# Kernel tuning notes

Measured on AMD Instinct MI355X. Metric: run time of the kernel, lower is better.

The kernel has to match this reference:

```python
import jax, jax.numpy as jnp
import numpy as np

N, E, D, H = 50000, 800000, 128, 4
EPS = 1e-5


def setup_inputs() -> dict:
    key = jax.random.key(0)
    ks = jax.random.split(key, 12)
    s_in = 1.0 / np.sqrt(D)
    s_att = 1.0 / np.sqrt(D)
    inp = {
        "x": jax.random.normal(ks[0], (N, D), dtype=jnp.float32),
        "edge_index": jax.random.randint(ks[1], (2, E), 0, N, dtype=jnp.int32),
        # conv1 params: W [D, H*D], att_src/att_dst [H, D], bias [D]
        "W1": jax.random.normal(ks[2], (D, H * D), dtype=jnp.float32) * s_in,
        "as1": jax.random.normal(ks[3], (H, D), dtype=jnp.float32) * s_att,
        "ad1": jax.random.normal(ks[4], (H, D), dtype=jnp.float32) * s_att,
        "b1": jnp.zeros((D,), dtype=jnp.float32),
        "g1": jnp.ones((D,), dtype=jnp.float32),
        "be1": jnp.zeros((D,), dtype=jnp.float32),
        # conv2 params
        "W2": jax.random.normal(ks[5], (D, H * D), dtype=jnp.float32) * s_in,
        "as2": jax.random.normal(ks[6], (H, D), dtype=jnp.float32) * s_att,
        "ad2": jax.random.normal(ks[7], (H, D), dtype=jnp.float32) * s_att,
        "b2": jnp.zeros((D,), dtype=jnp.float32),
        "g2": jnp.ones((D,), dtype=jnp.float32),
        "be2": jnp.zeros((D,), dtype=jnp.float32),
    }
    return inp


def _gat_conv(x, src, dst, W, att_src, att_dst, bias):
    # project: [N, H, C]
    h = (x @ W).reshape(N, H, D)
    a_src = jnp.einsum("nhc,hc->nh", h, att_src)  # [N, H]
    a_dst = jnp.einsum("nhc,hc->nh", h, att_dst)  # [N, H]
    # attention logits per edge, softmax over incoming edges of each dst
    logits = jax.nn.leaky_relu(a_src[src] + a_dst[dst], negative_slope=0.2)  # [Etot, H]
    lmax = jax.ops.segment_max(logits, dst, num_segments=N)  # [N, H]
    p = jnp.exp(logits - lmax[dst])
    denom = jax.ops.segment_sum(p, dst, num_segments=N)  # [N, H]
    alpha = p / denom[dst]  # self-loops guarantee denom > 0
    # weighted scatter-add aggregation
    msg = h[src] * alpha[:, :, None]  # [Etot, H, C]
    out = jax.ops.segment_sum(msg, dst, num_segments=N)  # [N, H, C]
    return out.mean(axis=1) + bias  # concat=False: mean over heads


def _batchnorm_relu(x, gamma, beta):
    mu = x.mean(axis=0)
    var = x.var(axis=0)  # biased, as torch uses for normalization
    xn = (x - mu) * jax.lax.rsqrt(var + EPS)
    return jax.nn.relu(xn * gamma + beta)


def reference(x, edge_index, W1, as1, ad1, b1, g1, be1, W2, as2, ad2, b2, g2, be2):
    # add self loops (GATConv default add_self_loops=True)
    loop = jnp.arange(N, dtype=edge_index.dtype)
    src = jnp.concatenate([edge_index[0], loop])
    dst = jnp.concatenate([edge_index[1], loop])
    x = _batchnorm_relu(_gat_conv(x, src, dst, W1, as1, ad1, b1), g1, be1)
    x = _batchnorm_relu(_gat_conv(x, src, dst, W2, as2, ad2, b2), g2, be2)
    return x
```

## Files before the change

kernel.cpp:

```cpp
#include <hip/hip_runtime.h>
#include <hip/hip_bf16.h>
#include <hip/hip_fp16.h>
#include <math.h>

#define NN 50000
#define NP 50048
#define NE 800000
#define ET (NE + NN)
#define DF 128
#define NH 4
#define HD 512
#define BN_EPS 1e-5f

typedef __hip_bfloat16 bf16;
typedef __attribute__((ext_vector_type(8))) short bf16x8;
typedef __attribute__((ext_vector_type(4))) float f32x4;

struct alignas(8) h2x2 { __half2 a, b; };

__global__ __launch_bounds__(256) void cvt_x_bf16(const float* __restrict__ in, bf16* __restrict__ out) {
    int i = blockIdx.x * 256 + threadIdx.x;
    if (i >= NN * DF / 4) return;
    float4 v = reinterpret_cast<const float4*>(in)[i];
    union { bf16 b[4]; short4 s; } u;
    u.b[0] = __float2bfloat16(v.x); u.b[1] = __float2bfloat16(v.y);
    u.b[2] = __float2bfloat16(v.z); u.b[3] = __float2bfloat16(v.w);
    reinterpret_cast<short4*>(out)[i] = u.s;
}

__global__ __launch_bounds__(256) void make_wsd(const float* __restrict__ W1, const float* __restrict__ as1,
                                                const float* __restrict__ ad1,
                                                const float* __restrict__ W2, const float* __restrict__ as2,
                                                const float* __restrict__ ad2,
                                                float* __restrict__ wsd) {
    int t = blockIdx.x * 256 + threadIdx.x;
    if (t >= 2048) return;
    int layer = t >> 10;
    int o = (t >> 7) & 7;
    int d = t & 127;
    int h = o & 3;
    const float* W  = layer ? W2 : W1;
    const float* av = layer ? (o < 4 ? as2 : ad2) : (o < 4 ? as1 : ad1);
    const float* wrow = W + d * HD + h * DF;
    const float* arow = av + h * DF;
    float sum = 0.f;
    for (int c = 0; c < DF; ++c) sum += wrow[c] * arow[c];
    wsd[layer * 1024 + o * DF + d] = sum;
}

__global__ __launch_bounds__(256) void cvt_bt2(const float* __restrict__ W1, const float* __restrict__ W2,
                                               bf16* __restrict__ B1, bf16* __restrict__ B2) {
    int i = blockIdx.x * 256 + threadIdx.x;
    if (i >= 2 * DF * HD) return;
    int layer = i >> 16;
    int ii = i & 65535;
    int c = ii >> 9, k = ii & 511;
    int h = k >> 7, d = k & 127;
    const float* W = layer ? W2 : W1;
    bf16* B = layer ? B2 : B1;
    B[ii] = __float2bfloat16(0.25f * W[d * HD + h * DF + c]);
}

__global__ __launch_bounds__(256) void xscore(const bf16* __restrict__ X,
                                              const float* __restrict__ wsd,
                                              float* __restrict__ a_src,
                                              float* __restrict__ a_dst) {
    __shared__ float w[8][DF];
    reinterpret_cast<float4*>(&w[0][0])[threadIdx.x] = reinterpret_cast<const float4*>(wsd)[threadIdx.x];
    __syncthreads();
    const int n = blockIdx.x * 4 + (threadIdx.x >> 6);
    const int l = threadIdx.x & 63;
    unsigned xv = reinterpret_cast<const unsigned*>(X)[n * 64 + l];
    float x0 = __uint_as_float(xv << 16);
    float x1 = __uint_as_float(xv & 0xffff0000u);
    float v[8];
    #pragma unroll
    for (int o = 0; o < 8; ++o)
        v[o] = x0 * w[o][2 * l] + x1 * w[o][2 * l + 1];
    #pragma unroll
    for (int off = 1; off < 64; off <<= 1) {
        #pragma unroll
        for (int o = 0; o < 8; ++o) v[o] += __shfl_xor(v[o], off);
    }
    if (l == 0) {
        reinterpret_cast<float4*>(a_src)[n] = make_float4(v[0], v[1], v[2], v[3]);
        reinterpret_cast<float4*>(a_dst)[n] = make_float4(v[4], v[5], v[6], v[7]);
    }
}

__global__ __launch_bounds__(256) void count_rank(const int* __restrict__ ei, int* __restrict__ counts,
                                                  int* __restrict__ rank) {
    int e = (blockIdx.x * 256 + threadIdx.x) * 2;
    if (e >= ET) return;
    int d0, d1;
    if (e + 1 < NE) {
        int2 dd = *reinterpret_cast<const int2*>(ei + NE + e);
        d0 = dd.x; d1 = dd.y;
    } else {
        d0 = (e < NE) ? ei[NE + e] : (e - NE);
        d1 = (e + 1 < NE) ? ei[NE + e + 1] : (e + 1 - NE);
    }
    rank[e]     = atomicAdd(&counts[d0 << 4], 1);
    rank[e + 1] = atomicAdd(&counts[d1 << 4], 1);
}

__global__ __launch_bounds__(256) void scan1(const int* __restrict__ counts, int* __restrict__ bsum) {
    __shared__ int sd[256];
    int i = blockIdx.x * 256 + threadIdx.x;
    sd[threadIdx.x] = (i < NN) ? counts[i << 4] : 0;
    __syncthreads();
    for (int s = 128; s > 0; s >>= 1) {
        if (threadIdx.x < s) sd[threadIdx.x] += sd[threadIdx.x + s];
        __syncthreads();
    }
    if (threadIdx.x == 0) bsum[blockIdx.x] = sd[0];
}

__global__ __launch_bounds__(256) void scan2(int* __restrict__ bsum, int nb) {
    __shared__ int sd[256];
    int i = threadIdx.x;
    int v = (i < nb) ? bsum[i] : 0;
    sd[i] = v;
    __syncthreads();
    for (int s = 1; s < 256; s <<= 1) {
        int t = sd[i];
        int u = (i >= s) ? sd[i - s] : 0;
        __syncthreads();
        sd[i] = t + u;
        __syncthreads();
    }
    if (i < nb) bsum[i] = sd[i] - v;
}

__global__ __launch_bounds__(256) void scan3(const int* __restrict__ counts, const int* __restrict__ bsum,
                                             int* __restrict__ row_ptr) {
    __shared__ int sd[256];
    int i = blockIdx.x * 256 + threadIdx.x;
    int v = (i < NN) ? counts[i << 4] : 0;
    sd[threadIdx.x] = v;
    __syncthreads();
    for (int s = 1; s < 256; s <<= 1) {
        int t = sd[threadIdx.x];
        int u = (threadIdx.x >= s) ? sd[threadIdx.x - s] : 0;
        __syncthreads();
        sd[threadIdx.x] = t + u;
        __syncthreads();
    }
    int excl = sd[threadIdx.x] - v + bsum[blockIdx.x];
    if (i < NN) row_ptr[i] = excl;
    if (i == 0) row_ptr[NN] = ET;
}

__global__ __launch_bounds__(256) void fill_scatter(const int* __restrict__ ei, const int* __restrict__ rank,
                                                    const int* __restrict__ row_ptr, int* __restrict__ col) {
    int e = (blockIdx.x * 256 + threadIdx.x) * 2;
    if (e >= ET) return;
    int s0, d0, s1, d1;
    if (e + 1 < NE) {
        int2 ss = *reinterpret_cast<const int2*>(ei + e);
        int2 dd = *reinterpret_cast<const int2*>(ei + NE + e);
        s0 = ss.x; s1 = ss.y; d0 = dd.x; d1 = dd.y;
    } else {
        if (e < NE) { s0 = ei[e]; d0 = ei[NE + e]; } else { s0 = d0 = e - NE; }
        if (e + 1 < NE) { s1 = ei[e + 1]; d1 = ei[NE + e + 1]; } else { s1 = d1 = e + 1 - NE; }
    }
    int2 rk = *reinterpret_cast<const int2*>(rank + e);
    col[row_ptr[d0] + rk.x] = s0;
    col[row_ptr[d1] + rk.y] = s1;
}

__global__ __launch_bounds__(256) void edge_alpha(const float* __restrict__ a_src,
                                                  const float* __restrict__ a_dst,
                                                  const int* __restrict__ row_ptr,
                                                  const int* __restrict__ col,
                                                  __half* __restrict__ alpha) {
    const int n = blockIdx.x * 4 + (threadIdx.x >> 6);
    const int l = threadIdx.x & 63;
    const int start = row_ptr[n], end = row_ptr[n + 1];
    const float4 ad4 = reinterpret_cast<const float4*>(a_dst)[n];
    const float4* __restrict__ as4 = reinterpret_cast<const float4*>(a_src);
    if (end - start <= 64) {
        const int j = start + l;
        float lv[4] = {-1e30f, -1e30f, -1e30f, -1e30f};
        if (j < end) {
            float4 a = as4[col[j]];
            lv[0] = a.x + ad4.x; lv[1] = a.y + ad4.y; lv[2] = a.z + ad4.z; lv[3] = a.w + ad4.w;
            #pragma unroll
            for (int h = 0; h < 4; ++h) lv[h] = lv[h] > 0.f ? lv[h] : 0.2f * lv[h];
        }
        float m[4], p[4], s[4];
        #pragma unroll
        for (int h = 0; h < 4; ++h) m[h] = lv[h];
        #pragma unroll
        for (int off = 1; off < 64; off <<= 1) {
            #pragma unroll
            for (int h = 0; h < 4; ++h) m[h] = fmaxf(m[h], __shfl_xor(m[h], off));
        }
        #pragma unroll
        for (int h = 0; h < 4; ++h) { p[h] = (j < end) ? __expf(lv[h] - m[h]) : 0.f; s[h] = p[h]; }
        #pragma unroll
        for (int off = 1; off < 64; off <<= 1) {
            #pragma unroll
            for (int h = 0; h < 4; ++h) s[h] += __shfl_xor(s[h], off);
        }
        if (j < end) {
            h2x2 o;
            o.a = __floats2half2_rn(p[0] / s[0], p[1] / s[1]);
            o.b = __floats2half2_rn(p[2] / s[2], p[3] / s[3]);
            reinterpret_cast<h2x2*>(alpha)[j] = o;
        }
    } else {
        float m[4] = {-1e30f, -1e30f, -1e30f, -1e30f}, s[4] = {0.f, 0.f, 0.f, 0.f};
        for (int base = start; base < end; base += 64) {
            const int j = base + l;
            float lv[4] = {-1e30f, -1e30f, -1e30f, -1e30f};
            if (j < end) {
                float4 a = as4[col[j]];
                lv[0] = a.x + ad4.x; lv[1] = a.y + ad4.y; lv[2] = a.z + ad4.z; lv[3] = a.w + ad4.w;
                #pragma unroll
                for (int h = 0; h < 4; ++h) lv[h] = lv[h] > 0.f ? lv[h] : 0.2f * lv[h];
            }
            float cm[4], cp[4];
            #pragma unroll
            for (int h = 0; h < 4; ++h) cm[h] = lv[h];
            #pragma unroll
            for (int off = 1; off < 64; off <<= 1) {
                #pragma unroll
                for (int h = 0; h < 4; ++h) cm[h] = fmaxf(cm[h], __shfl_xor(cm[h], off));
            }
            #pragma unroll
            for (int h = 0; h < 4; ++h) {
                float nm = fmaxf(m[h], cm[h]);
                cp[h] = (j < end) ? __expf(lv[h] - nm) : 0.f;
                s[h] *= __expf(m[h] - nm);
                m[h] = nm;
            }
            #pragma unroll
            for (int off = 1; off < 64; off <<= 1) {
                #pragma unroll
                for (int h = 0; h < 4; ++h) cp[h] += __shfl_xor(cp[h], off);
            }
            #pragma unroll
            for (int h = 0; h < 4; ++h) s[h] += cp[h];
        }
        for (int base = start; base < end; base += 64) {
            const int j = base + l;
            if (j < end) {
                float4 a = as4[col[j]];
                float v0 = a.x + ad4.x, v1 = a.y + ad4.y, v2 = a.z + ad4.z, v3 = a.w + ad4.w;
                v0 = v0 > 0.f ? v0 : 0.2f * v0; v1 = v1 > 0.f ? v1 : 0.2f * v1;
                v2 = v2 > 0.f ? v2 : 0.2f * v2; v3 = v3 > 0.f ? v3 : 0.2f * v3;
                h2x2 o;
                o.a = __floats2half2_rn(__expf(v0 - m[0]) / s[0], __expf(v1 - m[1]) / s[1]);
                o.b = __floats2half2_rn(__expf(v2 - m[2]) / s[2], __expf(v3 - m[3]) / s[3]);
                reinterpret_cast<h2x2*>(alpha)[j] = o;
            }
        }
    }
}

#define EDGE(xu, pu) {                                                               \
    float lo = __uint_as_float((xu) << 16);                                          \
    float hi = __uint_as_float((xu) & 0xffff0000u);                                  \
    float2 f01 = __half22float2(*reinterpret_cast<const __half2*>(&(pu).x));         \
    float2 f23 = __half22float2(*reinterpret_cast<const __half2*>(&(pu).y));         \
    acc[0][0] += f01.x * lo; acc[0][1] += f01.x * hi;                                \
    acc[1][0] += f01.y * lo; acc[1][1] += f01.y * hi;                                \
    acc[2][0] += f23.x * lo; acc[2][1] += f23.x * hi;                                \
    acc[3][0] += f23.y * lo; acc[3][1] += f23.y * hi; }

__global__ __launch_bounds__(256) void aggregate_x(const bf16* __restrict__ X,
                                                   const __half* __restrict__ alpha,
                                                   const int* __restrict__ row_ptr,
                                                   const int* __restrict__ col,
                                                   bf16* __restrict__ aggX) {
    const int n = blockIdx.x * 4 + (threadIdx.x >> 6);
    const int l = threadIdx.x & 63;
    const int start = row_ptr[n], end = row_ptr[n + 1];
    const unsigned* __restrict__ X4 = reinterpret_cast<const unsigned*>(X);
    float acc[4][2] = {};
    int j = start;
    for (; j + 4 <= end; j += 4) {
        int c0 = col[j], c1 = col[j + 1], c2 = col[j + 2], c3 = col[j + 3];
        unsigned x0 = X4[c0 * 64 + l];
        unsigned x1 = X4[c1 * 64 + l];
        unsigned x2 = X4[c2 * 64 + l];
        unsigned x3 = X4[c3 * 64 + l];
        uint2 p0 = *reinterpret_cast<const uint2*>(alpha + 4 * j);
        uint2 p1 = *reinterpret_cast<const uint2*>(alpha + 4 * (j + 1));
        uint2 p2 = *reinterpret_cast<const uint2*>(alpha + 4 * (j + 2));
        uint2 p3 = *reinterpret_cast<const uint2*>(alpha + 4 * (j + 3));
        EDGE(x0, p0) EDGE(x1, p1) EDGE(x2, p2) EDGE(x3, p3)
    }
    for (; j < end; ++j) {
        unsigned x0 = X4[col[j] * 64 + l];
        uint2 p0 = *reinterpret_cast<const uint2*>(alpha + 4 * j);
        EDGE(x0, p0)
    }
    unsigned* outp = reinterpret_cast<unsigned*>(aggX) + (size_t)n * 256;
    #pragma unroll
    for (int h = 0; h < 4; ++h) {
        union { bf16 b; unsigned short u; } plo, phi;
        plo.b = __float2bfloat16(acc[h][0]);
        phi.b = __float2bfloat16(acc[h][1]);
        outp[h * 64 + l] = (unsigned)plo.u | ((unsigned)phi.u << 16);
    }
}

__global__ __launch_bounds__(256) void gemm_out(const bf16* __restrict__ A,
                                                const bf16* __restrict__ Bt,
                                                const float* __restrict__ bias,
                                                bf16* __restrict__ outb,
                                                float* __restrict__ stats, int M) {
    __shared__ __align__(16) char Bs[65536];
    __shared__ float ssum[128], ssq[128];
    const int tid = threadIdx.x;
    if (tid < 128) { ssum[tid] = 0.f; ssq[tid] = 0.f; }
    const int m0 = blockIdx.x * 64;
    const char* Ab = (const char*)A + (size_t)m0 * 1024;
    const char* Bb = (const char*)Bt;
    auto stageB = [&](int ph) {
        #pragma unroll
        for (int i = 0; i < 16; ++i) {
            int d = (tid + i * 256) * 16;
            int c = d >> 9;
            int kb = d & 511;
            int src = c * 1024 + ph * 512 + (kb ^ ((c & 7) << 4));
            __builtin_amdgcn_global_load_lds(
                (const __attribute__((address_space(1))) void*)(Bb + src),
                (__attribute__((address_space(3))) void*)(Bs + d), 16, 0, 0);
        }
    };
    const int lane = tid & 63;
    const int wave = tid >> 6;
    const int wm = (wave & 1) * 32;
    const int wnb = (wave >> 1) * 64;
    const int lr = lane & 15;
    const int lkb = (lane >> 4) * 16;
    f32x4 acc[2][4] = {};
    const char* arow0 = Ab + (size_t)(wm + lr) * 1024 + lkb;
    const char* arow1 = Ab + (size_t)(wm + 16 + lr) * 1024 + lkb;
    stageB(0);
    #pragma unroll
    for (int ph = 0; ph < 2; ++ph) {
        __syncthreads();
        #pragma unroll 4
        for (int kk = 0; kk < 8; ++kk) {
            int kg = ph * 512 + kk * 64;
            bf16x8 a0 = *(const bf16x8*)(arow0 + kg);
            bf16x8 a1 = *(const bf16x8*)(arow1 + kg);
            int kb = kk * 64 + lkb;
            #pragma unroll
            for (int nf = 0; nf < 4; ++nf) {
                int c = wnb + nf * 16 + lr;
                bf16x8 b = *(const bf16x8*)(Bs + c * 512 + (kb ^ ((c & 7) << 4)));
                acc[0][nf] = __builtin_amdgcn_mfma_f32_16x16x32_bf16(a0, b, acc[0][nf], 0, 0, 0);
                acc[1][nf] = __builtin_amdgcn_mfma_f32_16x16x32_bf16(a1, b, acc[1][nf], 0, 0, 0);
            }
        }
        if (ph == 0) {
            __syncthreads();
            stageB(1);
        }
    }
    const int orow = (lane >> 4) * 4;
    float bcol[4];
    #pragma unroll
    for (int nf = 0; nf < 4; ++nf) bcol[nf] = bias[wnb + nf * 16 + lr];
    #pragma unroll
    for (int nf = 0; nf < 4; ++nf) {
        float cs = 0.f, cq = 0.f;
        int c = wnb + nf * 16 + lr;
        #pragma unroll
        for (int mi = 0; mi < 2; ++mi) {
            #pragma unroll
            for (int r = 0; r < 4; ++r) {
                int gr = m0 + wm + mi * 16 + orow + r;
                if (gr < M) {
                    float v = acc[mi][nf][r] + bcol[nf];
                    outb[(size_t)gr * DF + c] = __float2bfloat16(v);
                    cs += v; cq += v * v;
                }
            }
        }
        atomicAdd(&ssum[c], cs);
        atomicAdd(&ssq[c], cq);
    }
    __syncthreads();
    if (tid < 128) {
        atomicAdd(&stats[tid], ssum[tid]);
        atomicAdd(&stats[128 + tid], ssq[tid]);
    }
}

__device__ __forceinline__ void bn_core(const uint4 v, int c0, const float* stats,
                                        const float* gamma, const float* beta, float* o) {
    float xv[8];
    xv[0] = __uint_as_float(v.x << 16); xv[1] = __uint_as_float(v.x & 0xffff0000u);
    xv[2] = __uint_as_float(v.y << 16); xv[3] = __uint_as_float(v.y & 0xffff0000u);
    xv[4] = __uint_as_float(v.z << 16); xv[5] = __uint_as_float(v.z & 0xffff0000u);
    xv[6] = __uint_as_float(v.w << 16); xv[7] = __uint_as_float(v.w & 0xffff0000u);
    #pragma unroll
    for (int k = 0; k < 8; ++k) {
        int c = c0 + k;
        float mu = stats[c] * (1.f / NN);
        float var = stats[128 + c] * (1.f / NN) - mu * mu;
        o[k] = fmaxf((xv[k] - mu) * rsqrtf(var + BN_EPS) * gamma[c] + beta[c], 0.f);
    }
}

__global__ __launch_bounds__(256) void bn_apply_bf16(const bf16* __restrict__ x, const float* __restrict__ stats,
                                                     const float* __restrict__ gamma, const float* __restrict__ beta,
                                                     bf16* __restrict__ out) {
    int i = blockIdx.x * 256 + threadIdx.x;
    if (i >= NN * DF / 8) return;
    uint4 v = reinterpret_cast<const uint4*>(x)[i];
    float o[8];
    bn_core(v, (i * 8) & 127, stats, gamma, beta, o);
    uint4 w;
    unsigned short* wb = reinterpret_cast<unsigned short*>(&w);
    #pragma unroll
    for (int k = 0; k < 8; ++k) {
        union { bf16 b; unsigned short u; } t;
        t.b = __float2bfloat16(o[k]);
        wb[k] = t.u;
    }
    reinterpret_cast<uint4*>(out)[i] = w;
}

__global__ __launch_bounds__(256) void bn_apply_f32(const bf16* __restrict__ x, const float* __restrict__ stats,
                                                    const float* __restrict__ gamma, const float* __restrict__ beta,
                                                    float* __restrict__ out) {
    int i = blockIdx.x * 256 + threadIdx.x;
    if (i >= NN * DF / 8) return;
    uint4 v = reinterpret_cast<const uint4*>(x)[i];
    float o[8];
    bn_core(v, (i * 8) & 127, stats, gamma, beta, o);
    float4* op = reinterpret_cast<float4*>(out) + (size_t)i * 2;
    op[0] = make_float4(o[0], o[1], o[2], o[3]);
    op[1] = make_float4(o[4], o[5], o[6], o[7]);
}

extern "C" void kernel_launch(void* const* d_in, const int* in_sizes, int n_in,
                              void* d_out, int out_size, void* d_ws, size_t ws_size,
                              hipStream_t stream) {
    (void)in_sizes; (void)n_in; (void)out_size; (void)ws_size;
    const float* x   = (const float*)d_in[0];
    const int*   ei  = (const int*)d_in[1];
    const float* W1  = (const float*)d_in[2];
    const float* as1 = (const float*)d_in[3];
    const float* ad1 = (const float*)d_in[4];
    const float* b1  = (const float*)d_in[5];
    const float* g1  = (const float*)d_in[6];
    const float* be1 = (const float*)d_in[7];
    const float* W2  = (const float*)d_in[8];
    const float* as2 = (const float*)d_in[9];
    const float* ad2 = (const float*)d_in[10];
    const float* b2  = (const float*)d_in[11];
    const float* g2  = (const float*)d_in[12];
    const float* be2 = (const float*)d_in[13];
    float* out = (float*)d_out;

    char* ws = (char*)d_ws;
    size_t off = 0;
    auto alloc = [&](size_t bytes) -> void* {
        void* p = ws + off;
        off += (bytes + 255) & ~(size_t)255;
        return p;
    };
    bf16*   aggX    = (bf16*)alloc((size_t)NP * HD * 2);
    bf16*   xb      = (bf16*)alloc((size_t)NP * DF * 2);
    bf16*   Bt2a    = (bf16*)alloc((size_t)DF * HD * 2);
    bf16*   Bt2b    = (bf16*)alloc((size_t)DF * HD * 2);
    float*  wsd     = (float*)alloc(2 * 1024 * 4);
    float*  a_src   = (float*)alloc((size_t)NN * NH * 4);
    float*  a_dst   = (float*)alloc((size_t)NN * NH * 4);
    int*    row_ptr = (int*)alloc((size_t)(NN + 1) * 4);
    int*    bsum    = (int*)alloc(256 * 4);
    int*    colidx  = (int*)alloc((size_t)ET * 4);
    __half* alpha   = (__half*)alloc((size_t)ET * 8);
    bf16*   agg     = (bf16*)alloc((size_t)NN * DF * 2);
    float*  stats   = (float*)alloc(256 * 4);
    int*    counts  = (int*)agg;
    int*    rank    = (int*)((char*)agg + ((size_t)NP << 6));

    const int NB = (NN + 255) / 256;
    const int EB2 = (ET / 2 + 255) / 256;
    const int BNB = (NN * DF / 8 + 255) / 256;

    cvt_x_bf16<<<(NN * DF / 4 + 255) / 256, 256, 0, stream>>>(x, xb);
    make_wsd<<<8, 256, 0, stream>>>(W1, as1, ad1, W2, as2, ad2, wsd);
    cvt_bt2<<<(2 * DF * HD + 255) / 256, 256, 0, stream>>>(W1, W2, Bt2a, Bt2b);
    hipMemsetAsync(counts, 0, (size_t)NP << 6, stream);
    count_rank<<<EB2, 256, 0, stream>>>(ei, counts, rank);
    scan1<<<NB, 256, 0, stream>>>(counts, bsum);
    scan2<<<1, 256, 0, stream>>>(bsum, NB);
    scan3<<<NB, 256, 0, stream>>>(counts, bsum, row_ptr);
    fill_scatter<<<EB2, 256, 0, stream>>>(ei, rank, row_ptr, colidx);

    xscore<<<NN / 4, 256, 0, stream>>>(xb, wsd, a_src, a_dst);
    edge_alpha<<<NN / 4, 256, 0, stream>>>(a_src, a_dst, row_ptr, colidx, alpha);
    aggregate_x<<<NN / 4, 256, 0, stream>>>(xb, alpha, row_ptr, colidx, aggX);
    hipMemsetAsync(stats, 0, 256 * 4, stream);
    gemm_out<<<NP / 64, 256, 0, stream>>>(aggX, Bt2a, b1, agg, stats, NN);
    bn_apply_bf16<<<BNB, 256, 0, stream>>>(agg, stats, g1, be1, xb);

    xscore<<<NN / 4, 256, 0, stream>>>(xb, wsd + 1024, a_src, a_dst);
    edge_alpha<<<NN / 4, 256, 0, stream>>>(a_src, a_dst, row_ptr, colidx, alpha);
    aggregate_x<<<NN / 4, 256, 0, stream>>>(xb, alpha, row_ptr, colidx, aggX);
    hipMemsetAsync(stats, 0, 256 * 4, stream);
    gemm_out<<<NP / 64, 256, 0, stream>>>(aggX, Bt2b, b2, agg, stats, NN);
    bn_apply_f32<<<BNB, 256, 0, stream>>>(agg, stats, g2, be2, out);
}
```

Measured before the change: 390.4 us.

## Fuse edge softmax into aggregation with online softmax, drop alpha buffer

Merges the edge_alpha and aggregate_x kernels into one kernel. It computes attention logits per 64-edge chunk, keeps an online softmax with running max and sum, and accumulates weighted neighbor features in registers. Normalization happens once at the end. The lane layout changes to four edge groups of 16 lanes, each loading 16-byte feature vectors, which adds a cross-group shuffle reduction. It also folds the stats memset into xscore. The fused kernel removes the fp16 alpha round-trip and a kernel launch, at the cost of more registers (32 accumulators) and serialized per-edge inner loops that may reduce memory-level parallelism.

```diff
diff --git a/kernel.cpp b/kernel.cpp
--- a/kernel.cpp
+++ b/kernel.cpp
@@ -1,6 +1,5 @@
 #include <hip/hip_runtime.h>
 #include <hip/hip_bf16.h>
-#include <hip/hip_fp16.h>
 #include <math.h>
 
 #define NN 50000
@@ -15,8 +14,6 @@
 typedef __hip_bfloat16 bf16;
 typedef __attribute__((ext_vector_type(8))) short bf16x8;
 typedef __attribute__((ext_vector_type(4))) float f32x4;
-
-struct alignas(8) h2x2 { __half2 a, b; };
 
 __global__ __launch_bounds__(256) void cvt_x_bf16(const float* __restrict__ in, bf16* __restrict__ out) {
     int i = blockIdx.x * 256 + threadIdx.x;
@@ -64,7 +61,10 @@
 __global__ __launch_bounds__(256) void xscore(const bf16* __restrict__ X,
                                               const float* __restrict__ wsd,
                                               float* __restrict__ a_src,
-                                              float* __restrict__ a_dst) {
+                                              float* __restrict__ a_dst,
+                                              float* __restrict__ stats) {
+    if (blockIdx.x == 0 && threadIdx.x < 64)
+        reinterpret_cast<float4*>(stats)[threadIdx.x] = make_float4(0.f, 0.f, 0.f, 0.f);
     __shared__ float w[8][DF];
     reinterpret_cast<float4*>(&w[0][0])[threadIdx.x] = reinterpret_cast<const float4*>(wsd)[threadIdx.x];
     __syncthreads();
@@ -169,141 +169,109 @@
     col[row_ptr[d1] + rk.y] = s1;
 }
 
-__global__ __launch_bounds__(256) void edge_alpha(const float* __restrict__ a_src,
-                                                  const float* __restrict__ a_dst,
-                                                  const int* __restrict__ row_ptr,
-                                                  const int* __restrict__ col,
-                                                  __half* __restrict__ alpha) {
-    const int n = blockIdx.x * 4 + (threadIdx.x >> 6);
+__global__ __launch_bounds__(256) void agg_fused(const bf16* __restrict__ X,
+                                                 const float* __restrict__ a_src,
+                                                 const float* __restrict__ a_dst,
+                                                 const int* __restrict__ row_ptr,
+                                                 const int* __restrict__ col,
+                                                 bf16* __restrict__ aggX) {
+    __shared__ __align__(16) float4 pal[4][64];
+    __shared__ int pcol[4][64];
+    const int w = threadIdx.x >> 6;
+    const int n = blockIdx.x * 4 + w;
     const int l = threadIdx.x & 63;
+    const int g = l >> 4;
+    const int q = l & 15;
     const int start = row_ptr[n], end = row_ptr[n + 1];
     const float4 ad4 = reinterpret_cast<const float4*>(a_dst)[n];
     const float4* __restrict__ as4 = reinterpret_cast<const float4*>(a_src);
-    if (end - start <= 64) {
-        const int j = start + l;
+    const uint4* __restrict__ X16 = reinterpret_cast<const uint4*>(X);
+    float m[4] = {-1e30f, -1e30f, -1e30f, -1e30f};
+    float s[4] = {0.f, 0.f, 0.f, 0.f};
+    float acc[4][8] = {};
+    for (int base = start; base < end; base += 64) {
+        const int j = base + l;
+        const bool valid = j < end;
+        const int cj = valid ? col[j] : 0;
         float lv[4] = {-1e30f, -1e30f, -1e30f, -1e30f};
-        if (j < end) {
-            float4 a = as4[col[j]];
+        if (valid) {
+            float4 a = as4[cj];
             lv[0] = a.x + ad4.x; lv[1] = a.y + ad4.y; lv[2] = a.z + ad4.z; lv[3] = a.w + ad4.w;
             #pragma unroll
             for (int h = 0; h < 4; ++h) lv[h] = lv[h] > 0.f ? lv[h] : 0.2f * lv[h];
         }
-        float m[4], p[4], s[4];
-        #pragma unroll
-        for (int h = 0; h < 4; ++h) m[h] = lv[h];
+        float cm[4];
+        #pragma unroll
+        for (int h = 0; h < 4; ++h) cm[h] = lv[h];
         #pragma unroll
         for (int off = 1; off < 64; off <<= 1) {
             #pragma unroll
-            for (int h = 0; h < 4; ++h) m[h] = fmaxf(m[h], __shfl_xor(m[h], off));
-        }
-        #pragma unroll
-        for (int h = 0; h < 4; ++h) { p[h] = (j < end) ? __expf(lv[h] - m[h]) : 0.f; s[h] = p[h]; }
+            for (int h = 0; h < 4; ++h) cm[h] = fmaxf(cm[h], __shfl_xor(cm[h], off));
+        }
+        float p[4], ps[4];
+        #pragma unroll
+        for (int h = 0; h < 4; ++h) {
+            float nm = fmaxf(m[h], cm[h]);
+            float sc = __expf(m[h] - nm);
+            p[h] = valid ? __expf(lv[h] - nm) : 0.f;
+            s[h] *= sc;
+            #pragma unroll
+            for (int f = 0; f < 8; ++f) acc[h][f] *= sc;
+            m[h] = nm;
+            ps[h] = p[h];
+        }
         #pragma unroll
         for (int off = 1; off < 64; off <<= 1) {
             #pragma unroll
-            for (int h = 0; h < 4; ++h) s[h] += __shfl_xor(s[h], off);
-        }
-        if (j < end) {
-            h2x2 o;
-            o.a = __floats2half2_rn(p[0] / s[0], p[1] / s[1]);
-            o.b = __floats2half2_rn(p[2] / s[2], p[3] / s[3]);
-            reinterpret_cast<h2x2*>(alpha)[j] = o;
-        }
-    } else {
-        float m[4] = {-1e30f, -1e30f, -1e30f, -1e30f}, s[4] = {0.f, 0.f, 0.f, 0.f};
-        for (int base = start; base < end; base += 64) {
-            const int j = base + l;
-            float lv[4] = {-1e30f, -1e30f, -1e30f, -1e30f};
-            if (j < end) {
-                float4 a = as4[col[j]];
-                lv[0] = a.x + ad4.x; lv[1] = a.y + ad4.y; lv[2] = a.z + ad4.z; lv[3] = a.w + ad4.w;
-                #pragma unroll
-                for (int h = 0; h < 4; ++h) lv[h] = lv[h] > 0.f ? lv[h] : 0.2f * lv[h];
+            for (int h = 0; h < 4; ++h) ps[h] += __shfl_xor(ps[h], off);
+        }
+        #pragma unroll
+        for (int h = 0; h < 4; ++h) s[h] += ps[h];
+        pal[w][l] = make_float4(p[0], p[1], p[2], p[3]);
+        pcol[w][l] = cj;
+        __builtin_amdgcn_wave_barrier();
+        const int cnt = min(64, end - base);
+        for (int ee = 0; ee < cnt; ee += 4) {
+            int cc = pcol[w][ee + g];
+            float4 pa = pal[w][ee + g];
+            uint4 xv = X16[(size_t)cc * 16 + q];
+            float xf[8];
+            xf[0] = __uint_as_float(xv.x << 16); xf[1] = __uint_as_float(xv.x & 0xffff0000u);
+            xf[2] = __uint_as_float(xv.y << 16); xf[3] = __uint_as_float(xv.y & 0xffff0000u);
+            xf[4] = __uint_as_float(xv.z << 16); xf[5] = __uint_as_float(xv.z & 0xffff0000u);
+            xf[6] = __uint_as_float(xv.w << 16); xf[7] = __uint_as_float(xv.w & 0xffff0000u);
+            #pragma unroll
+            for (int f = 0; f < 8; ++f) {
+                acc[0][f] += pa.x * xf[f];
+                acc[1][f] += pa.y * xf[f];
+                acc[2][f] += pa.z * xf[f];
+                acc[3][f] += pa.w * xf[f];
             }
-            float cm[4], cp[4];
-            #pragma unroll
-            for (int h = 0; h < 4; ++h) cm[h] = lv[h];
-            #pragma unroll
-            for (int off = 1; off < 64; off <<= 1) {
-                #pragma unroll
-                for (int h = 0; h < 4; ++h) cm[h] = fmaxf(cm[h], __shfl_xor(cm[h], off));
+        }
+        __builtin_amdgcn_wave_barrier();
+    }
+    #pragma unroll
+    for (int h = 0; h < 4; ++h)
+        #pragma unroll
+        for (int f = 0; f < 8; ++f) {
+            acc[h][f] += __shfl_xor(acc[h][f], 16);
+            acc[h][f] += __shfl_xor(acc[h][f], 32);
+        }
+    if (l < 16) {
+        uint4* outp = reinterpret_cast<uint4*>(aggX) + (size_t)n * 64;
+        #pragma unroll
+        for (int h = 0; h < 4; ++h) {
+            float inv = 1.f / s[h];
+            uint4 wv;
+            unsigned short* wb = reinterpret_cast<unsigned short*>(&wv);
+            #pragma unroll
+            for (int f = 0; f < 8; ++f) {
+                union { bf16 b; unsigned short u; } t;
+                t.b = __float2bfloat16(acc[h][f] * inv);
+                wb[f] = t.u;
             }
-            #pragma unroll
-            for (int h = 0; h < 4; ++h) {
-                float nm = fmaxf(m[h], cm[h]);
-                cp[h] = (j < end) ? __expf(lv[h] - nm) : 0.f;
-                s[h] *= __expf(m[h] - nm);
-                m[h] = nm;
-            }
-            #pragma unroll
-            for (int off = 1; off < 64; off <<= 1) {
-                #pragma unroll
-                for (int h = 0; h < 4; ++h) cp[h] += __shfl_xor(cp[h], off);
-            }
-            #pragma unroll
-            for (int h = 0; h < 4; ++h) s[h] += cp[h];
-        }
-        for (int base = start; base < end; base += 64) {
-            const int j = base + l;
-            if (j < end) {
-                float4 a = as4[col[j]];
-                float v0 = a.x + ad4.x, v1 = a.y + ad4.y, v2 = a.z + ad4.z, v3 = a.w + ad4.w;
-                v0 = v0 > 0.f ? v0 : 0.2f * v0; v1 = v1 > 0.f ? v1 : 0.2f * v1;
-                v2 = v2 > 0.f ? v2 : 0.2f * v2; v3 = v3 > 0.f ? v3 : 0.2f * v3;
-                h2x2 o;
-                o.a = __floats2half2_rn(__expf(v0 - m[0]) / s[0], __expf(v1 - m[1]) / s[1]);
-                o.b = __floats2half2_rn(__expf(v2 - m[2]) / s[2], __expf(v3 - m[3]) / s[3]);
-                reinterpret_cast<h2x2*>(alpha)[j] = o;
-            }
-        }
-    }
-}
-
-#define EDGE(xu, pu) {                                                               \
-    float lo = __uint_as_float((xu) << 16);                                          \
-    float hi = __uint_as_float((xu) & 0xffff0000u);                                  \
-    float2 f01 = __half22float2(*reinterpret_cast<const __half2*>(&(pu).x));         \
-    float2 f23 = __half22float2(*reinterpret_cast<const __half2*>(&(pu).y));         \
-    acc[0][0] += f01.x * lo; acc[0][1] += f01.x * hi;                                \
-    acc[1][0] += f01.y * lo; acc[1][1] += f01.y * hi;                                \
-    acc[2][0] += f23.x * lo; acc[2][1] += f23.x * hi;                                \
-    acc[3][0] += f23.y * lo; acc[3][1] += f23.y * hi; }
-
-__global__ __launch_bounds__(256) void aggregate_x(const bf16* __restrict__ X,
-                                                   const __half* __restrict__ alpha,
-                                                   const int* __restrict__ row_ptr,
-                                                   const int* __restrict__ col,
-                                                   bf16* __restrict__ aggX) {
-    const int n = blockIdx.x * 4 + (threadIdx.x >> 6);
-    const int l = threadIdx.x & 63;
-    const int start = row_ptr[n], end = row_ptr[n + 1];
-    const unsigned* __restrict__ X4 = reinterpret_cast<const unsigned*>(X);
-    float acc[4][2] = {};
-    int j = start;
-    for (; j + 4 <= end; j += 4) {
-        int c0 = col[j], c1 = col[j + 1], c2 = col[j + 2], c3 = col[j + 3];
-        unsigned x0 = X4[c0 * 64 + l];
-        unsigned x1 = X4[c1 * 64 + l];
-        unsigned x2 = X4[c2 * 64 + l];
-        unsigned x3 = X4[c3 * 64 + l];
-        uint2 p0 = *reinterpret_cast<const uint2*>(alpha + 4 * j);
-        uint2 p1 = *reinterpret_cast<const uint2*>(alpha + 4 * (j + 1));
-        uint2 p2 = *reinterpret_cast<const uint2*>(alpha + 4 * (j + 2));
-        uint2 p3 = *reinterpret_cast<const uint2*>(alpha + 4 * (j + 3));
-        EDGE(x0, p0) EDGE(x1, p1) EDGE(x2, p2) EDGE(x3, p3)
-    }
-    for (; j < end; ++j) {
-        unsigned x0 = X4[col[j] * 64 + l];
-        uint2 p0 = *reinterpret_cast<const uint2*>(alpha + 4 * j);
-        EDGE(x0, p0)
-    }
-    unsigned* outp = reinterpret_cast<unsigned*>(aggX) + (size_t)n * 256;
-    #pragma unroll
-    for (int h = 0; h < 4; ++h) {
-        union { bf16 b; unsigned short u; } plo, phi;
-        plo.b = __float2bfloat16(acc[h][0]);
-        phi.b = __float2bfloat16(acc[h][1]);
-        outp[h * 64 + l] = (unsigned)plo.u | ((unsigned)phi.u << 16);
+            outp[h * 16 + q] = wv;
+        }
     }
 }
 
@@ -478,7 +446,6 @@
     int*    row_ptr = (int*)alloc((size_t)(NN + 1) * 4);
     int*    bsum    = (int*)alloc(256 * 4);
     int*    colidx  = (int*)alloc((size_t)ET * 4);
-    __half* alpha   = (__half*)alloc((size_t)ET * 8);
     bf16*   agg     = (bf16*)alloc((size_t)NN * DF * 2);
     float*  stats   = (float*)alloc(256 * 4);
     int*    counts  = (int*)agg;
@@ -498,17 +465,13 @@
     scan3<<<NB, 256, 0, stream>>>(counts, bsum, row_ptr);
     fill_scatter<<<EB2, 256, 0, stream>>>(ei, rank, row_ptr, colidx);
 
-    xscore<<<NN / 4, 256, 0, stream>>>(xb, wsd, a_src, a_dst);
-    edge_alpha<<<NN / 4, 256, 0, stream>>>(a_src, a_dst, row_ptr, colidx, alpha);
-    aggregate_x<<<NN / 4, 256, 0, stream>>>(xb, alpha, row_ptr, colidx, aggX);
-    hipMemsetAsync(stats, 0, 256 * 4, stream);
+    xscore<<<NN / 4, 256, 0, stream>>>(xb, wsd, a_src, a_dst, stats);
+    agg_fused<<<NN / 4, 256, 0, stream>>>(xb, a_src, a_dst, row_ptr, colidx, aggX);
     gemm_out<<<NP / 64, 256, 0, stream>>>(aggX, Bt2a, b1, agg, stats, NN);
     bn_apply_bf16<<<BNB, 256, 0, stream>>>(agg, stats, g1, be1, xb);
 
-    xscore<<<NN / 4, 256, 0, stream>>>(xb, wsd + 1024, a_src, a_dst);
-    edge_alpha<<<NN / 4, 256, 0, stream>>>(a_src, a_dst, row_ptr, colidx, alpha);
-    aggregate_x<<<NN / 4, 256, 0, stream>>>(xb, alpha, row_ptr, colidx, aggX);
-    hipMemsetAsync(stats, 0, 256 * 4, stream);
+    xscore<<<NN / 4, 256, 0, stream>>>(xb, wsd + 1024, a_src, a_dst, stats);
+    agg_fused<<<NN / 4, 256, 0, stream>>>(xb, a_src, a_dst, row_ptr, colidx, aggX);
     gemm_out<<<NP / 64, 256, 0, stream>>>(aggX, Bt2b, b2, agg, stats, NN);
     bn_apply_f32<<<BNB, 256, 0, stream>>>(agg, stats, g2, be2, out);
 }
```

Measured after the change: 400.5 us. 1.03x slower.

## Fuse conversion/BN into xscore, split GEMM columns, deterministic stats reduction

Applied to the files above, without the earlier changes.

Fuses the fp32-to-bf16 conversion of x into the first score kernel, and fuses layer-1 batchnorm+ReLU into the layer-2 score kernel, removing two elementwise passes over node features. The output GEMM is split across 4 column groups of 32 with a 32 KB B tile per block, which cuts LDS per block and the staging phases and raises the block count. Global stats atomics are replaced by per-block partials in scratch plus a single-block reduction kernel. The single-block reduce adds a serial step of about 800 iterations per thread, and the A tile is now re-read from global once per column group.

```diff
diff --git a/kernel.cpp b/kernel.cpp
--- a/kernel.cpp
+++ b/kernel.cpp
@@ -11,6 +11,7 @@
 #define NH 4
 #define HD 512
 #define BN_EPS 1e-5f
+#define MB 782
 
 typedef __hip_bfloat16 bf16;
 typedef __attribute__((ext_vector_type(8))) short bf16x8;
@@ -18,14 +19,11 @@
 
 struct alignas(8) h2x2 { __half2 a, b; };
 
-__global__ __launch_bounds__(256) void cvt_x_bf16(const float* __restrict__ in, bf16* __restrict__ out) {
-    int i = blockIdx.x * 256 + threadIdx.x;
-    if (i >= NN * DF / 4) return;
-    float4 v = reinterpret_cast<const float4*>(in)[i];
-    union { bf16 b[4]; short4 s; } u;
-    u.b[0] = __float2bfloat16(v.x); u.b[1] = __float2bfloat16(v.y);
-    u.b[2] = __float2bfloat16(v.z); u.b[3] = __float2bfloat16(v.w);
-    reinterpret_cast<short4*>(out)[i] = u.s;
+__device__ __forceinline__ float rbf(float x, unsigned short* bits) {
+    union { bf16 b; unsigned short u; } t;
+    t.b = __float2bfloat16(x);
+    *bits = t.u;
+    return __uint_as_float(((unsigned)t.u) << 16);
 }
 
 __global__ __launch_bounds__(256) void make_wsd(const float* __restrict__ W1, const float* __restrict__ as1,
@@ -61,18 +59,65 @@
     B[ii] = __float2bfloat16(0.25f * W[d * HD + h * DF + c]);
 }
 
-__global__ __launch_bounds__(256) void xscore(const bf16* __restrict__ X,
-                                              const float* __restrict__ wsd,
-                                              float* __restrict__ a_src,
-                                              float* __restrict__ a_dst) {
+__global__ __launch_bounds__(256) void cvt_xscore(const float* __restrict__ X,
+                                                  const float* __restrict__ wsd,
+                                                  bf16* __restrict__ xb,
+                                                  float* __restrict__ a_src,
+                                                  float* __restrict__ a_dst) {
     __shared__ float w[8][DF];
     reinterpret_cast<float4*>(&w[0][0])[threadIdx.x] = reinterpret_cast<const float4*>(wsd)[threadIdx.x];
     __syncthreads();
     const int n = blockIdx.x * 4 + (threadIdx.x >> 6);
     const int l = threadIdx.x & 63;
-    unsigned xv = reinterpret_cast<const unsigned*>(X)[n * 64 + l];
-    float x0 = __uint_as_float(xv << 16);
-    float x1 = __uint_as_float(xv & 0xffff0000u);
+    float2 xv = reinterpret_cast<const float2*>(X)[n * 64 + l];
+    unsigned short u0, u1;
+    float x0 = rbf(xv.x, &u0);
+    float x1 = rbf(xv.y, &u1);
+    reinterpret_cast<unsigned*>(xb)[n * 64 + l] = (unsigned)u0 | ((unsigned)u1 << 16);
+    float v[8];
+    #pragma unroll
+    for (int o = 0; o < 8; ++o)
+        v[o] = x0 * w[o][2 * l] + x1 * w[o][2 * l + 1];
+    #pragma unroll
+    for (int off = 1; off < 64; off <<= 1) {
+        #pragma unroll
+        for (int o = 0; o < 8; ++o) v[o] += __shfl_xor(v[o], off);
+    }
+    if (l == 0) {
+        reinterpret_cast<float4*>(a_src)[n] = make_float4(v[0], v[1], v[2], v[3]);
+        reinterpret_cast<float4*>(a_dst)[n] = make_float4(v[4], v[5], v[6], v[7]);
+    }
+}
+
+__global__ __launch_bounds__(256) void bn_xscore(const bf16* __restrict__ agg,
+                                                 const float* __restrict__ stats,
+                                                 const float* __restrict__ gamma,
+                                                 const float* __restrict__ beta,
+                                                 const float* __restrict__ wsd,
+                                                 bf16* __restrict__ xb,
+                                                 float* __restrict__ a_src,
+                                                 float* __restrict__ a_dst) {
+    __shared__ float w[8][DF];
+    __shared__ float sc[DF], sh[DF];
+    reinterpret_cast<float4*>(&w[0][0])[threadIdx.x] = reinterpret_cast<const float4*>(wsd)[threadIdx.x];
+    if (threadIdx.x < DF) {
+        int c = threadIdx.x;
+        float mu = stats[c] * (1.f / NN);
+        float var = stats[128 + c] * (1.f / NN) - mu * mu;
+        float scale = gamma[c] * rsqrtf(var + BN_EPS);
+        sc[c] = scale;
+        sh[c] = beta[c] - mu * scale;
+    }
+    __syncthreads();
+    const int n = blockIdx.x * 4 + (threadIdx.x >> 6);
+    const int l = threadIdx.x & 63;
+    unsigned u = reinterpret_cast<const unsigned*>(agg)[n * 64 + l];
+    float x0 = fmaxf(__uint_as_float(u << 16) * sc[2 * l] + sh[2 * l], 0.f);
+    float x1 = fmaxf(__uint_as_float(u & 0xffff0000u) * sc[2 * l + 1] + sh[2 * l + 1], 0.f);
+    unsigned short u0, u1;
+    x0 = rbf(x0, &u0);
+    x1 = rbf(x1, &u1);
+    reinterpret_cast<unsigned*>(xb)[n * 64 + l] = (unsigned)u0 | ((unsigned)u1 << 16);
     float v[8];
     #pragma unroll
     for (int o = 0; o < 8; ++o)
@@ -311,121 +356,78 @@
                                                 const bf16* __restrict__ Bt,
                                                 const float* __restrict__ bias,
                                                 bf16* __restrict__ outb,
-                                                float* __restrict__ stats, int M) {
-    __shared__ __align__(16) char Bs[65536];
-    __shared__ float ssum[128], ssq[128];
+                                                float* __restrict__ scratch, int M) {
+    __shared__ __align__(16) char Bs[32768];
+    __shared__ float ssum[32], ssq[32];
     const int tid = threadIdx.x;
-    if (tid < 128) { ssum[tid] = 0.f; ssq[tid] = 0.f; }
+    if (tid < 32) { ssum[tid] = 0.f; ssq[tid] = 0.f; }
     const int m0 = blockIdx.x * 64;
+    const int by = blockIdx.y;
     const char* Ab = (const char*)A + (size_t)m0 * 1024;
-    const char* Bb = (const char*)Bt;
-    auto stageB = [&](int ph) {
-        #pragma unroll
-        for (int i = 0; i < 16; ++i) {
-            int d = (tid + i * 256) * 16;
-            int c = d >> 9;
-            int kb = d & 511;
-            int src = c * 1024 + ph * 512 + (kb ^ ((c & 7) << 4));
-            __builtin_amdgcn_global_load_lds(
-                (const __attribute__((address_space(1))) void*)(Bb + src),
-                (__attribute__((address_space(3))) void*)(Bs + d), 16, 0, 0);
-        }
-    };
+    const char* Bb = (const char*)Bt + (size_t)by * 32768;
+    #pragma unroll
+    for (int i = 0; i < 8; ++i) {
+        int d = (tid + i * 256) * 16;
+        int c = d >> 10;
+        int kb = d & 1023;
+        __builtin_amdgcn_global_load_lds(
+            (const __attribute__((address_space(1))) void*)(Bb + c * 1024 + (kb ^ ((c & 7) << 4))),
+            (__attribute__((address_space(3))) void*)(Bs + d), 16, 0, 0);
+    }
     const int lane = tid & 63;
     const int wave = tid >> 6;
     const int wm = (wave & 1) * 32;
-    const int wnb = (wave >> 1) * 64;
+    const int wn = (wave >> 1) * 16;
     const int lr = lane & 15;
     const int lkb = (lane >> 4) * 16;
-    f32x4 acc[2][4] = {};
+    const int cl = wn + lr;
+    f32x4 acc[2] = {};
     const char* arow0 = Ab + (size_t)(wm + lr) * 1024 + lkb;
     const char* arow1 = Ab + (size_t)(wm + 16 + lr) * 1024 + lkb;
-    stageB(0);
-    #pragma unroll
-    for (int ph = 0; ph < 2; ++ph) {
-        __syncthreads();
-        #pragma unroll 4
-        for (int kk = 0; kk < 8; ++kk) {
-            int kg = ph * 512 + kk * 64;
-            bf16x8 a0 = *(const bf16x8*)(arow0 + kg);
-            bf16x8 a1 = *(const bf16x8*)(arow1 + kg);
-            int kb = kk * 64 + lkb;
-            #pragma unroll
-            for (int nf = 0; nf < 4; ++nf) {
-                int c = wnb + nf * 16 + lr;
-                bf16x8 b = *(const bf16x8*)(Bs + c * 512 + (kb ^ ((c & 7) << 4)));
-                acc[0][nf] = __builtin_amdgcn_mfma_f32_16x16x32_bf16(a0, b, acc[0][nf], 0, 0, 0);
-                acc[1][nf] = __builtin_amdgcn_mfma_f32_16x16x32_bf16(a1, b, acc[1][nf], 0, 0, 0);
+    __syncthreads();
+    #pragma unroll 4
+    for (int kk = 0; kk < 16; ++kk) {
+        int kg = kk * 64;
+        bf16x8 a0 = *(const bf16x8*)(arow0 + kg);
+        bf16x8 a1 = *(const bf16x8*)(arow1 + kg);
+        int kb = kg + lkb;
+        bf16x8 b = *(const bf16x8*)(Bs + cl * 1024 + (kb ^ ((cl & 7) << 4)));
+        acc[0] = __builtin_amdgcn_mfma_f32_16x16x32_bf16(a0, b, acc[0], 0, 0, 0);
+        acc[1] = __builtin_amdgcn_mfma_f32_16x16x32_bf16(a1, b, acc[1], 0, 0, 0);
+    }
+    const int orow = (lane >> 4) * 4;
+    const int gc = by * 32 + cl;
+    const float bc = bias[gc];
+    float cs = 0.f, cq = 0.f;
+    #pragma unroll
+    for (int mi = 0; mi < 2; ++mi) {
+        #pragma unroll
+        for (int r = 0; r < 4; ++r) {
+            int gr = m0 + wm + mi * 16 + orow + r;
+            if (gr < M) {
+                float v = acc[mi][r] + bc;
+                outb[(size_t)gr * DF + gc] = __float2bfloat16(v);
+                cs += v; cq += v * v;
             }
         }
-        if (ph == 0) {
-            __syncthreads();
-            stageB(1);
-        }
-    }
-    const int orow = (lane >> 4) * 4;
-    float bcol[4];
-    #pragma unroll
-    for (int nf = 0; nf < 4; ++nf) bcol[nf] = bias[wnb + nf * 16 + lr];
-    #pragma unroll
-    for (int nf = 0; nf < 4; ++nf) {
-        float cs = 0.f, cq = 0.f;
-        int c = wnb + nf * 16 + lr;
-        #pragma unroll
-        for (int mi = 0; mi < 2; ++mi) {
-            #pragma unroll
-            for (int r = 0; r < 4; ++r) {
-                int gr = m0 + wm + mi * 16 + orow + r;
-                if (gr < M) {
-                    float v = acc[mi][nf][r] + bcol[nf];
-                    outb[(size_t)gr * DF + c] = __float2bfloat16(v);
-                    cs += v; cq += v * v;
-                }
-            }
-        }
-        atomicAdd(&ssum[c], cs);
-        atomicAdd(&ssq[c], cq);
-    }
-    __syncthreads();
-    if (tid < 128) {
-        atomicAdd(&stats[tid], ssum[tid]);
-        atomicAdd(&stats[128 + tid], ssq[tid]);
-    }
-}
-
-__device__ __forceinline__ void bn_core(const uint4 v, int c0, const float* stats,
-                                        const float* gamma, const float* beta, float* o) {
-    float xv[8];
-    xv[0] = __uint_as_float(v.x << 16); xv[1] = __uint_as_float(v.x & 0xffff0000u);
-    xv[2] = __uint_as_float(v.y << 16); xv[3] = __uint_as_float(v.y & 0xffff0000u);
-    xv[4] = __uint_as_float(v.z << 16); xv[5] = __uint_as_float(v.z & 0xffff0000u);
-    xv[6] = __uint_as_float(v.w << 16); xv[7] = __uint_as_float(v.w & 0xffff0000u);
-    #pragma unroll
-    for (int k = 0; k < 8; ++k) {
-        int c = c0 + k;
-        float mu = stats[c] * (1.f / NN);
-        float var = stats[128 + c] * (1.f / NN) - mu * mu;
-        o[k] = fmaxf((xv[k] - mu) * rsqrtf(var + BN_EPS) * gamma[c] + beta[c], 0.f);
-    }
-}
-
-__global__ __launch_bounds__(256) void bn_apply_bf16(const bf16* __restrict__ x, const float* __restrict__ stats,
-                                                     const float* __restrict__ gamma, const float* __restrict__ beta,
-                                                     bf16* __restrict__ out) {
-    int i = blockIdx.x * 256 + threadIdx.x;
-    if (i >= NN * DF / 8) return;
-    uint4 v = reinterpret_cast<const uint4*>(x)[i];
-    float o[8];
-    bn_core(v, (i * 8) & 127, stats, gamma, beta, o);
-    uint4 w;
-    unsigned short* wb = reinterpret_cast<unsigned short*>(&w);
-    #pragma unroll
-    for (int k = 0; k < 8; ++k) {
-        union { bf16 b; unsigned short u; } t;
-        t.b = __float2bfloat16(o[k]);
-        wb[k] = t.u;
-    }
-    reinterpret_cast<uint4*>(out)[i] = w;
+    }
+    atomicAdd(&ssum[cl], cs);
+    atomicAdd(&ssq[cl], cq);
+    __syncthreads();
+    if (tid < 64)
+        scratch[((size_t)by * MB + blockIdx.x) * 64 + tid] = (tid < 32) ? ssum[tid] : ssq[tid - 32];
+}
+
+__global__ __launch_bounds__(256) void stats_reduce(const float* __restrict__ scratch,
+                                                    float* __restrict__ stats) {
+    int t = threadIdx.x;
+    int c = t & 127, kind = t >> 7;
+    const float* p = scratch + (size_t)(c >> 5) * MB * 64 + kind * 32 + (c & 31);
+    float s = 0.f;
+    int i = 0;
+    #pragma unroll 8
+    for (; i < MB; ++i) s += p[(size_t)i * 64];
+    stats[t] = s;
 }
 
 __global__ __launch_bounds__(256) void bn_apply_f32(const bf16* __restrict__ x, const float* __restrict__ stats,
@@ -434,8 +436,20 @@
     int i = blockIdx.x * 256 + threadIdx.x;
     if (i >= NN * DF / 8) return;
     uint4 v = reinterpret_cast<const uint4*>(x)[i];
+    float xv[8];
+    xv[0] = __uint_as_float(v.x << 16); xv[1] = __uint_as_float(v.x & 0xffff0000u);
+    xv[2] = __uint_as_float(v.y << 16); xv[3] = __uint_as_float(v.y & 0xffff0000u);
+    xv[4] = __uint_as_float(v.z << 16); xv[5] = __uint_as_float(v.z & 0xffff0000u);
+    xv[6] = __uint_as_float(v.w << 16); xv[7] = __uint_as_float(v.w & 0xffff0000u);
     float o[8];
-    bn_core(v, (i * 8) & 127, stats, gamma, beta, o);
+    int c0 = (i * 8) & 127;
+    #pragma unroll
+    for (int k = 0; k < 8; ++k) {
+        int c = c0 + k;
+        float mu = stats[c] * (1.f / NN);
+        float var = stats[128 + c] * (1.f / NN) - mu * mu;
+        o[k] = fmaxf((xv[k] - mu) * rsqrtf(var + BN_EPS) * gamma[c] + beta[c], 0.f);
+    }
     float4* op = reinterpret_cast<float4*>(out) + (size_t)i * 2;
     op[0] = make_float4(o[0], o[1], o[2], o[3]);
     op[1] = make_float4(o[4], o[5], o[6], o[7]);
@@ -481,14 +495,15 @@
     __half* alpha   = (__half*)alloc((size_t)ET * 8);
     bf16*   agg     = (bf16*)alloc((size_t)NN * DF * 2);
     float*  stats   = (float*)alloc(256 * 4);
+    float*  scratch = (float*)alloc((size_t)4 * MB * 64 * 4);
     int*    counts  = (int*)agg;
     int*    rank    = (int*)((char*)agg + ((size_t)NP << 6));
 
     const int NB = (NN + 255) / 256;
     const int EB2 = (ET / 2 + 255) / 256;
     const int BNB = (NN * DF / 8 + 255) / 256;
-
-    cvt_x_bf16<<<(NN * DF / 4 + 255) / 256, 256, 0, stream>>>(x, xb);
+    dim3 ggrid(MB, 4);
+
     make_wsd<<<8, 256, 0, stream>>>(W1, as1, ad1, W2, as2, ad2, wsd);
     cvt_bt2<<<(2 * DF * HD + 255) / 256, 256, 0, stream>>>(W1, W2, Bt2a, Bt2b);
     hipMemsetAsync(counts, 0, (size_t)NP << 6, stream);
@@ -498,17 +513,16 @@
     scan3<<<NB, 256, 0, stream>>>(counts, bsum, row_ptr);
     fill_scatter<<<EB2, 256, 0, stream>>>(ei, rank, row_ptr, colidx);
 
-    xscore<<<NN / 4, 256, 0, stream>>>(xb, wsd, a_src, a_dst);
+    cvt_xscore<<<NN / 4, 256, 0, stream>>>(x, wsd, xb, a_src, a_dst);
     edge_alpha<<<NN / 4, 256, 0, stream>>>(a_src, a_dst, row_ptr, colidx, alpha);
     aggregate_x<<<NN / 4, 256, 0, stream>>>(xb, alpha, row_ptr, colidx, aggX);
-    hipMemsetAsync(stats, 0, 256 * 4, stream);
-    gemm_out<<<NP / 64, 256, 0, stream>>>(aggX, Bt2a, b1, agg, stats, NN);
-    bn_apply_bf16<<<BNB, 256, 0, stream>>>(agg, stats, g1, be1, xb);
-
-    xscore<<<NN / 4, 256, 0, stream>>>(xb, wsd + 1024, a_src, a_dst);
+    gemm_out<<<ggrid, 256, 0, stream>>>(aggX, Bt2a, b1, agg, scratch, NN);
+    stats_reduce<<<1, 256, 0, stream>>>(scratch, stats);
+
+    bn_xscore<<<NN / 4, 256, 0, stream>>>(agg, stats, g1, be1, wsd + 1024, xb, a_src, a_dst);
     edge_alpha<<<NN / 4, 256, 0, stream>>>(a_src, a_dst, row_ptr, colidx, alpha);
     aggregate_x<<<NN / 4, 256, 0, stream>>>(xb, alpha, row_ptr, colidx, aggX);
-    hipMemsetAsync(stats, 0, 256 * 4, stream);
-    gemm_out<<<NP / 64, 256, 0, stream>>>(aggX, Bt2b, b2, agg, stats, NN);
+    gemm_out<<<ggrid, 256, 0, stream>>>(aggX, Bt2b, b2, agg, scratch, NN);
+    stats_reduce<<<1, 256, 0, stream>>>(scratch, stats);
     bn_apply_f32<<<BNB, 256, 0, stream>>>(agg, stats, g2, be2, out);
 }
```

Result: slower. 533.1 us (+36.6%).
